# Kernel tuning notes

Hardware: AMD Instinct MI355X
Metric: run time of the kernel (lower is better)

Reference implementation:

```python
import jax, jax.numpy as jnp
import numpy as np

H = 16        # num_attention_heads
KV = 4        # num_key_value_heads
DH = 128      # head_dim
THETA = 10000.0
MIN_VAL = -1000000000000000.0


def _rope_tables(L):
    # inv_freq: (DH/2,), positions: (L,)
    inv_freq = 1.0 / (THETA ** (jnp.arange(0, DH, 2, dtype=jnp.float32) / DH))
    pos = jnp.arange(L, dtype=jnp.float32)
    freq = pos[:, None] * inv_freq[None, :]          # (L, DH/2)
    emb = jnp.concatenate([freq, freq], axis=-1)      # (L, DH)
    return jnp.cos(emb), jnp.sin(emb)


def _apply_rope(x, cos, sin):
    # x: (B, h, L, DH); cos/sin: (L, DH)
    left = x[..., : DH // 2]
    right = -x[..., DH // 2 :]
    rot = jnp.concatenate([right, left], axis=-1)
    return x * cos[None, None] + rot * sin[None, None]


def setup_inputs() -> dict:
    key = jax.random.key(0)
    ks = jax.random.split(key, 5)
    B, L, D = 2, 2048, 2048
    s = 0.02
    return {
        "hidden_state": jax.random.normal(ks[0], (B, L, D), jnp.float32),
        "attention_mask": jnp.ones((B, L), jnp.int32),
        "Wq": jax.random.normal(ks[1], (H * DH, D), jnp.float32) * s,
        "Wk": jax.random.normal(ks[2], (KV * DH, D), jnp.float32) * s,
        "Wv": jax.random.normal(ks[3], (KV * DH, D), jnp.float32) * s,
        "Wo": jax.random.normal(ks[4], (D, D), jnp.float32) * s,
    }


def reference(hidden_state, attention_mask, Wq, Wk, Wv, Wo):
    B, L, D = hidden_state.shape
    cos, sin = _rope_tables(L)

    q = jnp.einsum('bld,ed->ble', hidden_state, Wq).reshape(B, L, H, DH).transpose(0, 2, 1, 3)
    k = jnp.einsum('bld,ed->ble', hidden_state, Wk).reshape(B, L, KV, DH).transpose(0, 2, 1, 3)
    v = jnp.einsum('bld,ed->ble', hidden_state, Wv).reshape(B, L, KV, DH).transpose(0, 2, 1, 3)

    q = _apply_rope(q, cos, sin)
    k = _apply_rope(k, cos, sin)

    # GQA: repeat each KV head H/KV times -> (B, H, L, DH)
    g = H // KV
    k = jnp.repeat(k, g, axis=1)
    v = jnp.repeat(v, g, axis=1)

    scores = jnp.einsum('bhqd,bhkd->bhqk', q, k) / np.sqrt(DH)  # (B,H,L,L)

    causal = jnp.triu(jnp.full((L, L), MIN_VAL, jnp.float32), k=1)[None, None]  # (1,1,L,L)
    pad = (attention_mask == 0)[:, None, None, :]  # (B,1,1,L)
    mask = jnp.where(pad, MIN_VAL, causal)
    scores = scores + mask

    attn = jax.nn.softmax(scores.astype(jnp.float32), axis=-1).astype(q.dtype)
    out = jnp.einsum('bhqk,bhkd->bhqd', attn, v)
    out = out.transpose(0, 2, 1, 3).reshape(B, L, H * DH)
    return jnp.einsum('ble,de->bld', out, Wo)
```

## Files before the change

### kernel.cpp

```cpp
#include <hip/hip_runtime.h>
#include <cstdint>
#include <cmath>


typedef __bf16 bf16_t;
typedef __bf16 bf16x8 __attribute__((ext_vector_type(8)));
typedef __bf16 bf16x4 __attribute__((ext_vector_type(4)));
typedef float  f32x4  __attribute__((ext_vector_type(4)));

#define HQ   16
#define HKV  4
#define GQA  4
#define DHD  128
#define BB   2
#define LL   2048
#define DDIM 2048
#define MINV (-1e15f)
#define QSC  0.12751744f

static __device__ __forceinline__ f32x4 mfma16(bf16x8 a, bf16x8 b, f32x4 c) {
  return __builtin_amdgcn_mfma_f32_16x16x32_bf16(a, b, c, 0, 0, 0);
}

static __device__ __forceinline__ f32x4 mfma16k16(bf16x4 a, bf16x4 b, f32x4 c) {
#if __has_builtin(__builtin_amdgcn_mfma_f32_16x16x16bf16_1k)
  typedef short s4 __attribute__((ext_vector_type(4)));
  union U { bf16x4 h; s4 s; };
  U ua, ub; ua.h = a; ub.h = b;
  return __builtin_amdgcn_mfma_f32_16x16x16bf16_1k(ua.s, ub.s, c, 0, 0, 0);
#elif __has_builtin(__builtin_amdgcn_mfma_f32_16x16x16_bf16)
  return __builtin_amdgcn_mfma_f32_16x16x16_bf16(a, b, c, 0, 0, 0);
#else
  f32x4 d;
  asm volatile("v_mfma_f32_16x16x16_bf16 %0, %1, %2, %3"
               : "=v"(d) : "v"(a), "v"(b), "v"(c));
  return d;
#endif
}

#if __has_builtin(__builtin_amdgcn_exp2f)
#define EXP2F(x) __builtin_amdgcn_exp2f(x)
#else
#define EXP2F(x) exp2f(x)
#endif

static __device__ __forceinline__ void gld16(const bf16_t* g, bf16_t* l) {
  __builtin_amdgcn_global_load_lds(
      (const __attribute__((address_space(1))) void*)g,
      (__attribute__((address_space(3))) void*)l,
      16, 0, 0);
}

struct CastArgs {
  const float* s[5];
  bf16_t* d[5];
  int n[5];
};

__global__ __launch_bounds__(256) void cast5_kernel(CastArgs a) {
  const int t = blockIdx.y;
  const int i8 = (blockIdx.x * 256 + threadIdx.x) * 8;
  if (i8 >= a.n[t]) return;
  const float4* s = (const float4*)(a.s[t] + i8);
  float4 x = s[0], y = s[1];
  bf16x8 o = {(bf16_t)x.x, (bf16_t)x.y, (bf16_t)x.z, (bf16_t)x.w,
              (bf16_t)y.x, (bf16_t)y.y, (bf16_t)y.z, (bf16_t)y.w};
  *(bf16x8*)(a.d[t] + i8) = o;
}

template <int STORE>
__global__ __launch_bounds__(256) void gemm_tile(const bf16_t* __restrict__ A,
                                                 const bf16_t* __restrict__ W,
                                                 void* __restrict__ C0,
                                                 bf16_t* __restrict__ Ck,
                                                 bf16_t* __restrict__ Cv,
                                                 int M, int N, int K) {
  __shared__ __align__(16) bf16_t As[128 * 32];
  __shared__ __align__(16) bf16_t Bs[128 * 32];
  const int tid  = threadIdx.x;
  const int lane = tid & 63;
  const int wave = tid >> 6;
  const int l15  = lane & 15;
  const int quad = lane >> 4;
  const int m0 = blockIdx.y * 128;
  const int n0 = blockIdx.x * 128;

  const int srow = wave * 32 + (lane >> 2);
  const int scol = (lane & 3) * 8;
  const bf16_t* ag = A + (size_t)(m0 + srow) * K + scol;
  const bf16_t* wg = W + (size_t)(n0 + srow) * K + scol;
  bf16_t* al = As + wave * 1024;
  bf16_t* bl = Bs + wave * 1024;

  const int wm = (wave >> 1) * 64;
  const int wn = (wave & 1) * 64;

  f32x4 acc[4][4];
#pragma unroll
  for (int mi = 0; mi < 4; mi++)
#pragma unroll
    for (int ni = 0; ni < 4; ni++) acc[mi][ni] = {0.f, 0.f, 0.f, 0.f};

  for (int k0 = 0; k0 < K; k0 += 32) {
    __syncthreads();
    gld16(ag + k0, al);
    gld16(ag + k0 + (size_t)16 * K, al + 512);
    gld16(wg + k0, bl);
    gld16(wg + k0 + (size_t)16 * K, bl + 512);
    __syncthreads();
    bf16x8 af[4], bfr[4];
#pragma unroll
    for (int mi = 0; mi < 4; mi++)
      af[mi] = *(const bf16x8*)(As + (wm + mi * 16 + l15) * 32 + quad * 8);
#pragma unroll
    for (int ni = 0; ni < 4; ni++)
      bfr[ni] = *(const bf16x8*)(Bs + (wn + ni * 16 + l15) * 32 + quad * 8);
#pragma unroll
    for (int mi = 0; mi < 4; mi++)
#pragma unroll
      for (int ni = 0; ni < 4; ni++)
        acc[mi][ni] = mfma16(af[mi], bfr[ni], acc[mi][ni]);
  }

  if (STORE == 2) {
    float* C = (float*)C0;
#pragma unroll
    for (int mi = 0; mi < 4; mi++) {
      const int row = m0 + wm + mi * 16 + quad * 4;
#pragma unroll
      for (int ni = 0; ni < 4; ni++) {
        const int col = n0 + wn + ni * 16 + l15;
#pragma unroll
        for (int i = 0; i < 4; i++)
          C[(size_t)(row + i) * N + col] = acc[mi][ni][i];
      }
    }
  } else {
    if (n0 < 2048) {
      bf16_t* C = (bf16_t*)C0;
#pragma unroll
      for (int mi = 0; mi < 4; mi++) {
        const int row = m0 + wm + mi * 16 + quad * 4;
#pragma unroll
        for (int ni = 0; ni < 4; ni++) {
          const int col = n0 + wn + ni * 16 + l15;
#pragma unroll
          for (int i = 0; i < 4; i++)
            C[(size_t)(row + i) * 2048 + col] = (bf16_t)acc[mi][ni][i];
        }
      }
    } else if (n0 < 2560) {
#pragma unroll
      for (int mi = 0; mi < 4; mi++) {
        const int row = m0 + wm + mi * 16 + quad * 4;
#pragma unroll
        for (int ni = 0; ni < 4; ni++) {
          const int col = n0 - 2048 + wn + ni * 16 + l15;
#pragma unroll
          for (int i = 0; i < 4; i++)
            Ck[(size_t)(row + i) * 512 + col] = (bf16_t)acc[mi][ni][i];
        }
      }
    } else {
#pragma unroll
      for (int mi = 0; mi < 4; mi++) {
        const int row = m0 + wm + mi * 16 + quad * 4;
        const int b = row >> 11;
        const int l0 = row & (LL - 1);
#pragma unroll
        for (int ni = 0; ni < 4; ni++) {
          const int kvcol = n0 - 2560 + wn + ni * 16 + l15;
          const int kvh = kvcol >> 7, d = kvcol & 127;
          bf16x4 w4 = {(bf16_t)acc[mi][ni][0], (bf16_t)acc[mi][ni][1],
                       (bf16_t)acc[mi][ni][2], (bf16_t)acc[mi][ni][3]};
          *(bf16x4*)(Cv + ((size_t)(b * HKV + kvh) * DHD + d) * LL + l0) = w4;
        }
      }
    }
  }
}

__global__ void rope_kernel(bf16_t* __restrict__ q, bf16_t* __restrict__ k,
                            const int* __restrict__ amask, float* __restrict__ bias) {
  const int nq = BB * LL * HQ * 64;
  const int nk = BB * LL * HKV * 64;
  int id = blockIdx.x * blockDim.x + threadIdx.x;
  if (id >= nq + nk) {
    int id2 = id - (nq + nk);
    if (id2 < BB * LL) bias[id2] = (amask[id2] == 0) ? MINV : 0.0f;
    return;
  }
  bf16_t* base;
  int heads, idx;
  float sc;
  if (id < nq) { base = q; heads = HQ; idx = id; sc = QSC; }
  else         { base = k; heads = HKV; idx = id - nq; sc = 1.0f; }
  int d = idx & 63; idx >>= 6;
  int hh = idx % heads;
  int bl = idx / heads;
  int l = bl & (LL - 1);
  bf16_t* p = base + ((size_t)bl * heads + hh) * DHD + d;
  float x1 = (float)p[0];
  float x2 = (float)p[64];
  float invf = __expf(-(float)d * 0.14391156862532788f);
  float fr = (float)l * invf;
  float s, c;
  __sincosf(fr, &s, &c);
  p[0]  = (bf16_t)((x1 * c - x2 * s) * sc);
  p[64] = (bf16_t)((x2 * c + x1 * s) * sc);
}

__global__ __launch_bounds__(256, 2) void flash_attn2(const bf16_t* __restrict__ q,
                                                      const bf16_t* __restrict__ k,
                                                      const bf16_t* __restrict__ vt,
                                                      const float* __restrict__ bias,
                                                      bf16_t* __restrict__ o) {
  __shared__ __align__(16) bf16_t Kbuf[64 * 128];
  __shared__ __align__(16) bf16_t Vbuf[128 * 64];

  const int tid  = threadIdx.x;
  const int lane = tid & 63;
  const int wave = tid >> 6;
  const int l15  = lane & 15;
  const int quad = lane >> 4;

  const int bi   = blockIdx.x;
  const int half = bi >> 8;
  const int jj   = bi & 255;
  const int cc   = jj >> 5;
  const int c    = half ? (15 - cc) : cc;
  const int bh = jj & 31;
  const int b  = bh >> 4;
  const int h  = bh & 15;
  const int kv = h >> 2;

  const int q0[2] = { c * 64 + wave * 16, (31 - c) * 64 + wave * 16 };
  const int nrounds = 32 - c;

  bf16x8 qf[2][4];
#pragma unroll
  for (int qt = 0; qt < 2; qt++) {
    const bf16_t* qb = q + ((size_t)(b * LL + q0[qt] + l15)) * (HQ * DHD) + h * DHD + quad * 8;
#pragma unroll
    for (int t = 0; t < 4; t++) qf[qt][t] = *(const bf16x8*)(qb + 32 * t);
  }

  f32x4 acc[8][2];
#pragma unroll
  for (int mt = 0; mt < 8; mt++)
#pragma unroll
    for (int qt = 0; qt < 2; qt++) acc[mt][qt] = {0.f, 0.f, 0.f, 0.f};
  float m_i[2] = {-1e30f, -1e30f};
  float l_i[2] = {0.f, 0.f};

  const bf16_t* kg_base = k + ((size_t)(b * LL)) * (HKV * DHD) + kv * DHD;
  const bf16_t* vg_base = vt + ((size_t)(b * HKV + kv) * DHD) * LL;
  const float*  bias_b  = bias + b * LL;

  const int krow = tid >> 4, kch = tid & 15;
  const int vrow = tid >> 3, vch = tid & 7;
  const int vc0  = ((vch >> 2) << 5) + (((vch << 1) & 3) << 3) + (((vch >> 1) & 1) << 2);
  const int vblo = vc0 * 2;
  const int ksw  = (krow & 7) << 4;
  const int vsw  = (vrow & 7) << 4;
  const int rsw  = (l15 & 7) << 4;

  for (int r = 0; r < nrounds; r++) {
    const int j0 = r * 64;
    {
      const bf16_t* kg = kg_base + (size_t)(j0 + krow) * (HKV * DHD) + kch * 8;
      const bf16_t* vg = vg_base + (size_t)vrow * LL + j0 + vch * 8;
      bf16x8 kl[4], vl[4];
#pragma unroll
      for (int p = 0; p < 4; p++) kl[p] = *(const bf16x8*)(kg + (size_t)p * 16 * (HKV * DHD));
#pragma unroll
      for (int p = 0; p < 4; p++) vl[p] = *(const bf16x8*)(vg + (size_t)p * 32 * LL);
      __syncthreads();
#pragma unroll
      for (int p = 0; p < 4; p++)
        *(bf16x8*)((char*)Kbuf + (size_t)(krow + p * 16) * 256 + ((kch * 16) ^ ksw)) = kl[p];
#pragma unroll
      for (int p = 0; p < 4; p++) {
        char* vbase = (char*)Vbuf + (size_t)(vrow + p * 32) * 128;
        bf16x4 lo4 = __builtin_shufflevector(vl[p], vl[p], 0, 1, 2, 3);
        bf16x4 hi4 = __builtin_shufflevector(vl[p], vl[p], 4, 5, 6, 7);
        *(bf16x4*)(vbase + (vblo ^ vsw)) = lo4;
        *(bf16x4*)(vbase + ((vblo + 16) ^ vsw)) = hi4;
      }
      __syncthreads();
    }
    const bool act_a = (r <= c);

    f32x4 s[2][4];
#pragma unroll
    for (int kt = 0; kt < 4; kt++) {
      const char* kr = (const char*)Kbuf + (size_t)(kt * 16 + l15) * 256;
      f32x4 s0 = {0.f, 0.f, 0.f, 0.f};
      f32x4 s1 = {0.f, 0.f, 0.f, 0.f};
#pragma unroll
      for (int t = 0; t < 4; t++) {
        bf16x8 kf = *(const bf16x8*)(kr + ((quad * 16 + t * 64) ^ rsw));
        if (act_a) s0 = mfma16(kf, qf[0][t], s0);
        s1 = mfma16(kf, qf[1][t], s1);
      }
      s[0][kt] = s0; s[1][kt] = s1;
    }

    f32x4 bv[4];
#pragma unroll
    for (int kt = 0; kt < 4; kt++) bv[kt] = *(const f32x4*)(bias_b + j0 + kt * 16 + quad * 4);

    bf16x4 pf[2][4];
#pragma unroll
    for (int qt = 0; qt < 2; qt++) {
      if (qt == 0 && !act_a) continue;
      const int qrow = q0[qt] + l15;
      const bool diag = (j0 + 63 > q0[qt]);
      float mx = -1e30f;
#pragma unroll
      for (int kt = 0; kt < 4; kt++) {
        f32x4 sv = s[qt][kt];
#pragma unroll
        for (int i = 0; i < 4; i++) {
          float x = sv[i] + bv[kt][i];
          if (diag) {
            int key = j0 + kt * 16 + quad * 4 + i;
            if (key > qrow) x = MINV;
          }
          sv[i] = x;
          mx = fmaxf(mx, x);
        }
        s[qt][kt] = sv;
      }
      mx = fmaxf(mx, __shfl_xor(mx, 16));
      mx = fmaxf(mx, __shfl_xor(mx, 32));
      if (!__all(mx <= m_i[qt] + 8.0f)) {
        const float mn = fmaxf(m_i[qt], mx);
        const float alpha = EXP2F(m_i[qt] - mn);
        m_i[qt] = mn;
        l_i[qt] *= alpha;
#pragma unroll
        for (int mt = 0; mt < 8; mt++) {
          acc[mt][qt][0] *= alpha; acc[mt][qt][1] *= alpha;
          acc[mt][qt][2] *= alpha; acc[mt][qt][3] *= alpha;
        }
      }
      const float mn = m_i[qt];
      float sum = 0.f;
#pragma unroll
      for (int kt = 0; kt < 4; kt++) {
        f32x4 sv = s[qt][kt];
        bf16x4 p4;
#pragma unroll
        for (int i = 0; i < 4; i++) {
          float p = EXP2F(sv[i] - mn);
          sum += p;
          p4[i] = (bf16_t)p;
        }
        pf[qt][kt] = p4;
      }
      sum += __shfl_xor(sum, 16);
      sum += __shfl_xor(sum, 32);
      l_i[qt] += sum;
    }

#pragma unroll
    for (int mt = 0; mt < 8; mt++) {
      const char* vr = (const char*)Vbuf + (size_t)(mt * 16 + l15) * 128;
      bf16x8 v01 = *(const bf16x8*)(vr + ((quad * 16) ^ rsw));
      bf16x8 v23 = *(const bf16x8*)(vr + ((64 + quad * 16) ^ rsw));
      bf16x4 va = __builtin_shufflevector(v01, v01, 0, 1, 2, 3);
      bf16x4 vb = __builtin_shufflevector(v01, v01, 4, 5, 6, 7);
      bf16x4 vc = __builtin_shufflevector(v23, v23, 0, 1, 2, 3);
      bf16x4 vd = __builtin_shufflevector(v23, v23, 4, 5, 6, 7);
      if (act_a) {
        acc[mt][0] = mfma16k16(va, pf[0][0], acc[mt][0]);
        acc[mt][0] = mfma16k16(vb, pf[0][1], acc[mt][0]);
        acc[mt][0] = mfma16k16(vc, pf[0][2], acc[mt][0]);
        acc[mt][0] = mfma16k16(vd, pf[0][3], acc[mt][0]);
      }
      acc[mt][1] = mfma16k16(va, pf[1][0], acc[mt][1]);
      acc[mt][1] = mfma16k16(vb, pf[1][1], acc[mt][1]);
      acc[mt][1] = mfma16k16(vc, pf[1][2], acc[mt][1]);
      acc[mt][1] = mfma16k16(vd, pf[1][3], acc[mt][1]);
    }
  }

#pragma unroll
  for (int qt = 0; qt < 2; qt++) {
    const float invl = 1.0f / l_i[qt];
    bf16_t* ob = o + ((size_t)(b * LL + q0[qt] + l15)) * (HQ * DHD) + h * DHD + quad * 4;
#pragma unroll
    for (int mt = 0; mt < 8; mt++) {
      f32x4 a = acc[mt][qt];
      bf16x4 w = {(bf16_t)(a[0] * invl), (bf16_t)(a[1] * invl),
                  (bf16_t)(a[2] * invl), (bf16_t)(a[3] * invl)};
      *(bf16x4*)(ob + mt * 16) = w;
    }
  }
}

extern "C" void kernel_launch(void* const* d_in, const int* in_sizes, int n_in,
                              void* d_out, int out_size, void* d_ws, size_t ws_size,
                              hipStream_t stream) {
  const float* hidden = (const float*)d_in[0];
  const int*   amask  = (const int*)d_in[1];
  const float* Wq     = (const float*)d_in[2];
  const float* Wk     = (const float*)d_in[3];
  const float* Wv     = (const float*)d_in[4];
  const float* Wo     = (const float*)d_in[5];
  float* out = (float*)d_out;

  const int M = BB * LL;
  const size_t MB = 1u << 20;
  char* ws = (char*)d_ws;
  bf16_t* hid_b   = (bf16_t*)(ws);
  bf16_t* q_ws    = (bf16_t*)(ws + 16 * MB);
  bf16_t* attn_ws = (bf16_t*)(ws + 32 * MB);
  bf16_t* k_ws    = (bf16_t*)(ws + 48 * MB);
  bf16_t* vt_ws   = (bf16_t*)(ws + 52 * MB);
  bf16_t* wqkv_b  = (bf16_t*)(ws + 56 * MB);
  bf16_t* wq_b    = wqkv_b;
  bf16_t* wk_b    = (bf16_t*)(ws + 64 * MB);
  bf16_t* wv_b    = (bf16_t*)(ws + 66 * MB);
  bf16_t* wo_b    = (bf16_t*)(ws + 68 * MB);
  float*  bias_ws = (float*)(ws);

  CastArgs ca;
  ca.s[0] = hidden; ca.d[0] = hid_b; ca.n[0] = BB * LL * DDIM;
  ca.s[1] = Wq;     ca.d[1] = wq_b;  ca.n[1] = HQ * DHD * DDIM;
  ca.s[2] = Wk;     ca.d[2] = wk_b;  ca.n[2] = HKV * DHD * DDIM;
  ca.s[3] = Wv;     ca.d[3] = wv_b;  ca.n[3] = HKV * DHD * DDIM;
  ca.s[4] = Wo;     ca.d[4] = wo_b;  ca.n[4] = DDIM * DDIM;
  {
    int maxn = BB * LL * DDIM;
    dim3 g((maxn / 8 + 255) / 256, 5);
    cast5_kernel<<<g, 256, 0, stream>>>(ca);
  }

  gemm_tile<3><<<dim3(3072 / 128, M / 128), 256, 0, stream>>>(
      hid_b, wqkv_b, q_ws, k_ws, vt_ws, M, 3072, DDIM);

  {
    int total = BB * LL * (HQ + HKV) * 64 + BB * LL;
    rope_kernel<<<(total + 255) / 256, 256, 0, stream>>>(q_ws, k_ws, amask, bias_ws);
  }

  flash_attn2<<<BB * HQ * 16, 256, 0, stream>>>(q_ws, k_ws, vt_ws, bias_ws, attn_ws);

  gemm_tile<2><<<dim3(DDIM / 128, M / 128), 256, 0, stream>>>(
      attn_ws, wo_b, (void*)out, nullptr, nullptr, M, DDIM, DDIM);
}
```

Measured before the change: 344.0 us.

## Double-buffer K/V tiles in LDS with register prefetch and cache bias in shared memory

Converts the flash-attention K/V staging to a two-buffer LDS scheme. The global loads for the tile two steps ahead are issued into registers while the current tile computes, and the next tile is written to the alternate buffer, so each round needs one barrier instead of two. The key-padding bias row is copied into shared memory once per block. s_setprio is raised around the MFMA sections. LDS use grows to about 72KB per block, which may lower occupancy under launch_bounds(256,2), and register pressure rises from the in-flight prefetch.

Result: slower. 375.7 us (+9.2%).

```diff
diff --git a/kernel.cpp b/kernel.cpp
--- a/kernel.cpp
+++ b/kernel.cpp
@@ -215,8 +215,9 @@
                                                       const bf16_t* __restrict__ vt,
                                                       const float* __restrict__ bias,
                                                       bf16_t* __restrict__ o) {
-  __shared__ __align__(16) bf16_t Kbuf[64 * 128];
-  __shared__ __align__(16) bf16_t Vbuf[128 * 64];
+  __shared__ __align__(16) bf16_t Kbuf[2][64 * 128];
+  __shared__ __align__(16) bf16_t Vbuf[2][128 * 64];
+  __shared__ __align__(16) float  Bb[2048];
 
   const int tid  = threadIdx.x;
   const int lane = tid & 63;
@@ -257,6 +258,13 @@
   const bf16_t* vg_base = vt + ((size_t)(b * HKV + kv) * DHD) * LL;
   const float*  bias_b  = bias + b * LL;
 
+  {
+    const float4* bs = (const float4*)bias_b;
+    float4* bd = (float4*)Bb;
+    bd[tid]       = bs[tid];
+    bd[tid + 256] = bs[tid + 256];
+  }
+
   const int krow = tid >> 4, kch = tid & 15;
   const int vrow = tid >> 3, vch = tid & 7;
   const int vc0  = ((vch >> 2) << 5) + (((vch << 1) & 3) << 3) + (((vch >> 1) & 1) << 2);
@@ -265,36 +273,53 @@
   const int vsw  = (vrow & 7) << 4;
   const int rsw  = (l15 & 7) << 4;
 
+  const bf16_t* kg0 = kg_base + (size_t)krow * (HKV * DHD) + kch * 8;
+  const bf16_t* vg0 = vg_base + (size_t)vrow * LL + vch * 8;
+
+  bf16x8 kl[4], vl[4];
+  auto ISSUE = [&](int j0) {
+#pragma unroll
+    for (int p = 0; p < 4; p++)
+      kl[p] = *(const bf16x8*)(kg0 + (size_t)j0 * (HKV * DHD) + (size_t)p * 16 * (HKV * DHD));
+#pragma unroll
+    for (int p = 0; p < 4; p++)
+      vl[p] = *(const bf16x8*)(vg0 + j0 + (size_t)p * 32 * LL);
+  };
+  auto STAGE = [&](int bsel) {
+    char* kb = (char*)(&Kbuf[bsel][0]);
+    char* vb = (char*)(&Vbuf[bsel][0]);
+#pragma unroll
+    for (int p = 0; p < 4; p++)
+      *(bf16x8*)(kb + (size_t)(krow + p * 16) * 256 + ((kch * 16) ^ ksw)) = kl[p];
+#pragma unroll
+    for (int p = 0; p < 4; p++) {
+      char* vbase = vb + (size_t)(vrow + p * 32) * 128;
+      bf16x4 lo4 = __builtin_shufflevector(vl[p], vl[p], 0, 1, 2, 3);
+      bf16x4 hi4 = __builtin_shufflevector(vl[p], vl[p], 4, 5, 6, 7);
+      *(bf16x4*)(vbase + (vblo ^ vsw)) = lo4;
+      *(bf16x4*)(vbase + ((vblo + 16) ^ vsw)) = hi4;
+    }
+  };
+
+  ISSUE(0);
+  STAGE(0);
+  ISSUE(64);
+  asm volatile("s_waitcnt lgkmcnt(0)" ::: "memory");
+  __builtin_amdgcn_s_barrier();
+  __builtin_amdgcn_sched_barrier(0);
+
+  int cur = 0;
   for (int r = 0; r < nrounds; r++) {
     const int j0 = r * 64;
-    {
-      const bf16_t* kg = kg_base + (size_t)(j0 + krow) * (HKV * DHD) + kch * 8;
-      const bf16_t* vg = vg_base + (size_t)vrow * LL + j0 + vch * 8;
-      bf16x8 kl[4], vl[4];
-#pragma unroll
-      for (int p = 0; p < 4; p++) kl[p] = *(const bf16x8*)(kg + (size_t)p * 16 * (HKV * DHD));
-#pragma unroll
-      for (int p = 0; p < 4; p++) vl[p] = *(const bf16x8*)(vg + (size_t)p * 32 * LL);
-      __syncthreads();
-#pragma unroll
-      for (int p = 0; p < 4; p++)
-        *(bf16x8*)((char*)Kbuf + (size_t)(krow + p * 16) * 256 + ((kch * 16) ^ ksw)) = kl[p];
-#pragma unroll
-      for (int p = 0; p < 4; p++) {
-        char* vbase = (char*)Vbuf + (size_t)(vrow + p * 32) * 128;
-        bf16x4 lo4 = __builtin_shufflevector(vl[p], vl[p], 0, 1, 2, 3);
-        bf16x4 hi4 = __builtin_shufflevector(vl[p], vl[p], 4, 5, 6, 7);
-        *(bf16x4*)(vbase + (vblo ^ vsw)) = lo4;
-        *(bf16x4*)(vbase + ((vblo + 16) ^ vsw)) = hi4;
-      }
-      __syncthreads();
-    }
     const bool act_a = (r <= c);
+    const char* KbC = (const char*)(&Kbuf[cur][0]);
+    const char* VbC = (const char*)(&Vbuf[cur][0]);
 
     f32x4 s[2][4];
+    __builtin_amdgcn_s_setprio(1);
 #pragma unroll
     for (int kt = 0; kt < 4; kt++) {
-      const char* kr = (const char*)Kbuf + (size_t)(kt * 16 + l15) * 256;
+      const char* kr = KbC + (size_t)(kt * 16 + l15) * 256;
       f32x4 s0 = {0.f, 0.f, 0.f, 0.f};
       f32x4 s1 = {0.f, 0.f, 0.f, 0.f};
 #pragma unroll
@@ -305,10 +330,7 @@
       }
       s[0][kt] = s0; s[1][kt] = s1;
     }
-
-    f32x4 bv[4];
-#pragma unroll
-    for (int kt = 0; kt < 4; kt++) bv[kt] = *(const f32x4*)(bias_b + j0 + kt * 16 + quad * 4);
+    __builtin_amdgcn_s_setprio(0);
 
     bf16x4 pf[2][4];
 #pragma unroll
@@ -320,9 +342,10 @@
 #pragma unroll
       for (int kt = 0; kt < 4; kt++) {
         f32x4 sv = s[qt][kt];
+        f32x4 bv = *(const f32x4*)(&Bb[j0 + kt * 16 + quad * 4]);
 #pragma unroll
         for (int i = 0; i < 4; i++) {
-          float x = sv[i] + bv[kt][i];
+          float x = sv[i] + bv[i];
           if (diag) {
             int key = j0 + kt * 16 + quad * 4 + i;
             if (key > qrow) x = MINV;
@@ -364,9 +387,10 @@
       l_i[qt] += sum;
     }
 
+    __builtin_amdgcn_s_setprio(1);
 #pragma unroll
     for (int mt = 0; mt < 8; mt++) {
-      const char* vr = (const char*)Vbuf + (size_t)(mt * 16 + l15) * 128;
+      const char* vr = VbC + (size_t)(mt * 16 + l15) * 128;
       bf16x8 v01 = *(const bf16x8*)(vr + ((quad * 16) ^ rsw));
       bf16x8 v23 = *(const bf16x8*)(vr + ((64 + quad * 16) ^ rsw));
       bf16x4 va = __builtin_shufflevector(v01, v01, 0, 1, 2, 3);
@@ -383,6 +407,16 @@
       acc[mt][1] = mfma16k16(vb, pf[1][1], acc[mt][1]);
       acc[mt][1] = mfma16k16(vc, pf[1][2], acc[mt][1]);
       acc[mt][1] = mfma16k16(vd, pf[1][3], acc[mt][1]);
+    }
+    __builtin_amdgcn_s_setprio(0);
+
+    if (r + 1 < nrounds) {
+      STAGE(cur ^ 1);
+      if (r + 2 < nrounds) ISSUE((r + 2) * 64);
+      asm volatile("s_waitcnt lgkmcnt(0)" ::: "memory");
+      __builtin_amdgcn_s_barrier();
+      __builtin_amdgcn_sched_barrier(0);
+      cur ^= 1;
     }
   }
 
```

## Split flash attention blocks into per-wave 32-row paired tiles

Applied to the files above, without the earlier changes.

Reorganizes the attention kernel so each block handles two 32-row query tiles (p and 63-p), with waves 0-1 on one tile and waves 2-3 on the other, each wave owning a single 16-row slice. The grid doubles to 1024 blocks and per-wave accumulator state is halved, aiming to cut register pressure, raise occupancy and improve load balance. Inactive waves skip compute for rounds past their causal limit. In exchange, K/V tiles are loaded to LDS twice as often per query row, and idle waves still wait at barriers.

Result: faster. 330.2 us (-4.0%).

```diff
diff --git a/kernel.cpp b/kernel.cpp
--- a/kernel.cpp
+++ b/kernel.cpp
@@ -224,34 +224,31 @@
   const int l15  = lane & 15;
   const int quad = lane >> 4;
 
-  const int bi   = blockIdx.x;
-  const int half = bi >> 8;
-  const int jj   = bi & 255;
-  const int cc   = jj >> 5;
-  const int c    = half ? (15 - cc) : cc;
-  const int bh = jj & 31;
+  const int gi = blockIdx.x;
+  const int g  = gi >> 8;
+  const int j  = gi & 255;
+  const int p  = (j >> 5) + 8 * g;
+  const int bh = j & 31;
   const int b  = bh >> 4;
   const int h  = bh & 15;
   const int kv = h >> 2;
 
-  const int q0[2] = { c * 64 + wave * 16, (31 - c) * 64 + wave * 16 };
-  const int nrounds = 32 - c;
-
-  bf16x8 qf[2][4];
-#pragma unroll
-  for (int qt = 0; qt < 2; qt++) {
-    const bf16_t* qb = q + ((size_t)(b * LL + q0[qt] + l15)) * (HQ * DHD) + h * DHD + quad * 8;
-#pragma unroll
-    for (int t = 0; t < 4; t++) qf[qt][t] = *(const bf16x8*)(qb + 32 * t);
-  }
-
-  f32x4 acc[8][2];
-#pragma unroll
-  for (int mt = 0; mt < 8; mt++)
-#pragma unroll
-    for (int qt = 0; qt < 2; qt++) acc[mt][qt] = {0.f, 0.f, 0.f, 0.f};
-  float m_i[2] = {-1e30f, -1e30f};
-  float l_i[2] = {0.f, 0.f};
+  const int tile = (wave < 2) ? p : (63 - p);
+  const int q0   = tile * 32 + (wave & 1) * 16;
+  const int nrounds = 32 - (p >> 1);
+
+  bf16x8 qf[4];
+  {
+    const bf16_t* qb = q + ((size_t)(b * LL + q0 + l15)) * (HQ * DHD) + h * DHD + quad * 8;
+#pragma unroll
+    for (int t = 0; t < 4; t++) qf[t] = *(const bf16x8*)(qb + 32 * t);
+  }
+
+  f32x4 acc[8];
+#pragma unroll
+  for (int mt = 0; mt < 8; mt++) acc[mt] = {0.f, 0.f, 0.f, 0.f};
+  float m_i = -1e30f;
+  float l_i = 0.f;
 
   const bf16_t* kg_base = k + ((size_t)(b * LL)) * (HKV * DHD) + kv * DHD;
   const bf16_t* vg_base = vt + ((size_t)(b * HKV + kv) * DHD) * LL;
@@ -272,57 +269,49 @@
       const bf16_t* vg = vg_base + (size_t)vrow * LL + j0 + vch * 8;
       bf16x8 kl[4], vl[4];
 #pragma unroll
-      for (int p = 0; p < 4; p++) kl[p] = *(const bf16x8*)(kg + (size_t)p * 16 * (HKV * DHD));
-#pragma unroll
-      for (int p = 0; p < 4; p++) vl[p] = *(const bf16x8*)(vg + (size_t)p * 32 * LL);
+      for (int pp = 0; pp < 4; pp++) kl[pp] = *(const bf16x8*)(kg + (size_t)pp * 16 * (HKV * DHD));
+#pragma unroll
+      for (int pp = 0; pp < 4; pp++) vl[pp] = *(const bf16x8*)(vg + (size_t)pp * 32 * LL);
       __syncthreads();
 #pragma unroll
-      for (int p = 0; p < 4; p++)
-        *(bf16x8*)((char*)Kbuf + (size_t)(krow + p * 16) * 256 + ((kch * 16) ^ ksw)) = kl[p];
-#pragma unroll
-      for (int p = 0; p < 4; p++) {
-        char* vbase = (char*)Vbuf + (size_t)(vrow + p * 32) * 128;
-        bf16x4 lo4 = __builtin_shufflevector(vl[p], vl[p], 0, 1, 2, 3);
-        bf16x4 hi4 = __builtin_shufflevector(vl[p], vl[p], 4, 5, 6, 7);
+      for (int pp = 0; pp < 4; pp++)
+        *(bf16x8*)((char*)Kbuf + (size_t)(krow + pp * 16) * 256 + ((kch * 16) ^ ksw)) = kl[pp];
+#pragma unroll
+      for (int pp = 0; pp < 4; pp++) {
+        char* vbase = (char*)Vbuf + (size_t)(vrow + pp * 32) * 128;
+        bf16x4 lo4 = __builtin_shufflevector(vl[pp], vl[pp], 0, 1, 2, 3);
+        bf16x4 hi4 = __builtin_shufflevector(vl[pp], vl[pp], 4, 5, 6, 7);
         *(bf16x4*)(vbase + (vblo ^ vsw)) = lo4;
         *(bf16x4*)(vbase + ((vblo + 16) ^ vsw)) = hi4;
       }
       __syncthreads();
     }
-    const bool act_a = (r <= c);
-
-    f32x4 s[2][4];
-#pragma unroll
-    for (int kt = 0; kt < 4; kt++) {
-      const char* kr = (const char*)Kbuf + (size_t)(kt * 16 + l15) * 256;
-      f32x4 s0 = {0.f, 0.f, 0.f, 0.f};
-      f32x4 s1 = {0.f, 0.f, 0.f, 0.f};
-#pragma unroll
-      for (int t = 0; t < 4; t++) {
-        bf16x8 kf = *(const bf16x8*)(kr + ((quad * 16 + t * 64) ^ rsw));
-        if (act_a) s0 = mfma16(kf, qf[0][t], s0);
-        s1 = mfma16(kf, qf[1][t], s1);
-      }
-      s[0][kt] = s0; s[1][kt] = s1;
-    }
-
-    f32x4 bv[4];
-#pragma unroll
-    for (int kt = 0; kt < 4; kt++) bv[kt] = *(const f32x4*)(bias_b + j0 + kt * 16 + quad * 4);
-
-    bf16x4 pf[2][4];
-#pragma unroll
-    for (int qt = 0; qt < 2; qt++) {
-      if (qt == 0 && !act_a) continue;
-      const int qrow = q0[qt] + l15;
-      const bool diag = (j0 + 63 > q0[qt]);
+
+    const bool act = (j0 <= q0 + 15);
+    if (act) {
+      f32x4 s[4];
+#pragma unroll
+      for (int kt = 0; kt < 4; kt++) {
+        const char* kr = (const char*)Kbuf + (size_t)(kt * 16 + l15) * 256;
+        f32x4 s0 = {0.f, 0.f, 0.f, 0.f};
+#pragma unroll
+        for (int t = 0; t < 4; t++) {
+          bf16x8 kf = *(const bf16x8*)(kr + ((quad * 16 + t * 64) ^ rsw));
+          s0 = mfma16(kf, qf[t], s0);
+        }
+        s[kt] = s0;
+      }
+
+      const int qrow = q0 + l15;
+      const bool diag = (j0 + 63 > q0);
       float mx = -1e30f;
 #pragma unroll
       for (int kt = 0; kt < 4; kt++) {
-        f32x4 sv = s[qt][kt];
+        f32x4 sv = s[kt];
+        f32x4 bv = *(const f32x4*)(bias_b + j0 + kt * 16 + quad * 4);
 #pragma unroll
         for (int i = 0; i < 4; i++) {
-          float x = sv[i] + bv[kt][i];
+          float x = sv[i] + bv[i];
           if (diag) {
             int key = j0 + kt * 16 + quad * 4 + i;
             if (key > qrow) x = MINV;
@@ -330,69 +319,63 @@
           sv[i] = x;
           mx = fmaxf(mx, x);
         }
-        s[qt][kt] = sv;
+        s[kt] = sv;
       }
       mx = fmaxf(mx, __shfl_xor(mx, 16));
       mx = fmaxf(mx, __shfl_xor(mx, 32));
-      if (!__all(mx <= m_i[qt] + 8.0f)) {
-        const float mn = fmaxf(m_i[qt], mx);
-        const float alpha = EXP2F(m_i[qt] - mn);
-        m_i[qt] = mn;
-        l_i[qt] *= alpha;
+      if (!__all(mx <= m_i + 8.0f)) {
+        const float mn = fmaxf(m_i, mx);
+        const float alpha = EXP2F(m_i - mn);
+        m_i = mn;
+        l_i *= alpha;
 #pragma unroll
         for (int mt = 0; mt < 8; mt++) {
-          acc[mt][qt][0] *= alpha; acc[mt][qt][1] *= alpha;
-          acc[mt][qt][2] *= alpha; acc[mt][qt][3] *= alpha;
-        }
-      }
-      const float mn = m_i[qt];
+          acc[mt][0] *= alpha; acc[mt][1] *= alpha;
+          acc[mt][2] *= alpha; acc[mt][3] *= alpha;
+        }
+      }
+      const float mn = m_i;
       float sum = 0.f;
+      bf16x4 pf[4];
 #pragma unroll
       for (int kt = 0; kt < 4; kt++) {
-        f32x4 sv = s[qt][kt];
+        f32x4 sv = s[kt];
         bf16x4 p4;
 #pragma unroll
         for (int i = 0; i < 4; i++) {
-          float p = EXP2F(sv[i] - mn);
-          sum += p;
-          p4[i] = (bf16_t)p;
-        }
-        pf[qt][kt] = p4;
+          float pe = EXP2F(sv[i] - mn);
+          sum += pe;
+          p4[i] = (bf16_t)pe;
+        }
+        pf[kt] = p4;
       }
       sum += __shfl_xor(sum, 16);
       sum += __shfl_xor(sum, 32);
-      l_i[qt] += sum;
+      l_i += sum;
+
+#pragma unroll
+      for (int mt = 0; mt < 8; mt++) {
+        const char* vr = (const char*)Vbuf + (size_t)(mt * 16 + l15) * 128;
+        bf16x8 v01 = *(const bf16x8*)(vr + ((quad * 16) ^ rsw));
+        bf16x8 v23 = *(const bf16x8*)(vr + ((64 + quad * 16) ^ rsw));
+        bf16x4 va = __builtin_shufflevector(v01, v01, 0, 1, 2, 3);
+        bf16x4 vb = __builtin_shufflevector(v01, v01, 4, 5, 6, 7);
+        bf16x4 vc = __builtin_shufflevector(v23, v23, 0, 1, 2, 3);
+        bf16x4 vd = __builtin_shufflevector(v23, v23, 4, 5, 6, 7);
+        acc[mt] = mfma16k16(va, pf[0], acc[mt]);
+        acc[mt] = mfma16k16(vb, pf[1], acc[mt]);
+        acc[mt] = mfma16k16(vc, pf[2], acc[mt]);
+        acc[mt] = mfma16k16(vd, pf[3], acc[mt]);
+      }
     }
-
+  }
+
+  {
+    const float invl = 1.0f / l_i;
+    bf16_t* ob = o + ((size_t)(b * LL + q0 + l15)) * (HQ * DHD) + h * DHD + quad * 4;
 #pragma unroll
     for (int mt = 0; mt < 8; mt++) {
-      const char* vr = (const char*)Vbuf + (size_t)(mt * 16 + l15) * 128;
-      bf16x8 v01 = *(const bf16x8*)(vr + ((quad * 16) ^ rsw));
-      bf16x8 v23 = *(const bf16x8*)(vr + ((64 + quad * 16) ^ rsw));
-      bf16x4 va = __builtin_shufflevector(v01, v01, 0, 1, 2, 3);
-      bf16x4 vb = __builtin_shufflevector(v01, v01, 4, 5, 6, 7);
-      bf16x4 vc = __builtin_shufflevector(v23, v23, 0, 1, 2, 3);
-      bf16x4 vd = __builtin_shufflevector(v23, v23, 4, 5, 6, 7);
-      if (act_a) {
-        acc[mt][0] = mfma16k16(va, pf[0][0], acc[mt][0]);
-        acc[mt][0] = mfma16k16(vb, pf[0][1], acc[mt][0]);
-        acc[mt][0] = mfma16k16(vc, pf[0][2], acc[mt][0]);
-        acc[mt][0] = mfma16k16(vd, pf[0][3], acc[mt][0]);
-      }
-      acc[mt][1] = mfma16k16(va, pf[1][0], acc[mt][1]);
-      acc[mt][1] = mfma16k16(vb, pf[1][1], acc[mt][1]);
-      acc[mt][1] = mfma16k16(vc, pf[1][2], acc[mt][1]);
-      acc[mt][1] = mfma16k16(vd, pf[1][3], acc[mt][1]);
-    }
-  }
-
-#pragma unroll
-  for (int qt = 0; qt < 2; qt++) {
-    const float invl = 1.0f / l_i[qt];
-    bf16_t* ob = o + ((size_t)(b * LL + q0[qt] + l15)) * (HQ * DHD) + h * DHD + quad * 4;
-#pragma unroll
-    for (int mt = 0; mt < 8; mt++) {
-      f32x4 a = acc[mt][qt];
+      f32x4 a = acc[mt];
       bf16x4 w = {(bf16_t)(a[0] * invl), (bf16_t)(a[1] * invl),
                   (bf16_t)(a[2] * invl), (bf16_t)(a[3] * invl)};
       *(bf16x4*)(ob + mt * 16) = w;
@@ -446,7 +429,7 @@
     rope_kernel<<<(total + 255) / 256, 256, 0, stream>>>(q_ws, k_ws, amask, bias_ws);
   }
 
-  flash_attn2<<<BB * HQ * 16, 256, 0, stream>>>(q_ws, k_ws, vt_ws, bias_ws, attn_ws);
+  flash_attn2<<<1024, 256, 0, stream>>>(q_ws, k_ws, vt_ws, bias_ws, attn_ws);
 
   gemm_tile<2><<<dim3(DDIM / 128, M / 128), 256, 0, stream>>>(
       attn_ws, wo_b, (void*)out, nullptr, nullptr, M, DDIM, DDIM);
```
